# Optimization experiments

Hardware: AMD Instinct MI355X
Metric: run time of the kernel (lower is better)

## Reference

```python
import jax, jax.numpy as jnp
import numpy as np

KERNEL_SIZE = 3
STRIDE = 1

def setup_inputs() -> dict:
    key = jax.random.key(0)
    kx, kw, kb = jax.random.split(key, 3)
    B, C_in, L = 32, 64, 16384
    C_out = 64
    x = jax.random.normal(kx, (B, C_in, L), dtype=jnp.float32)
    # original uses torch.rand (uniform [0,1)) for params
    weight = jax.random.uniform(kw, (C_out, C_in, KERNEL_SIZE), dtype=jnp.float32)
    bias = jax.random.uniform(kb, (C_out,), dtype=jnp.float32)
    return {"x": x, "weight": weight, "bias": bias}

def reference(x, weight, bias):
    # x: (B, C_in, L), weight: (C_out, C_in, K) -> out: (B, C_out, L_out)
    out = jax.lax.conv_general_dilated(
        x, weight,
        window_strides=(STRIDE,),
        padding="VALID",
        dimension_numbers=("NCH", "OIH", "NCH"),
    )
    return out + bias[None, :, None]
```

## Files before the change

### kernel.cpp

```cpp
#include <hip/hip_runtime.h>


typedef __bf16 bf16x8 __attribute__((ext_vector_type(8)));
typedef unsigned short ushort8 __attribute__((ext_vector_type(8)));
typedef float f32x16 __attribute__((ext_vector_type(16)));

#define C_IN 64
#define C_OUT 64
#define L_IN 16384
#define L_OUT 16382
#define NT 256
#define PX 264
#define PW 200

__device__ __forceinline__ unsigned short f2bf(float f) {
  unsigned u = __builtin_bit_cast(unsigned, f);
  return (unsigned short)((u + 0x7FFFu + ((u >> 16) & 1u)) >> 16);
}

__global__ __launch_bounds__(256, 2) void conv1d_mfma(
    const float* __restrict__ x, const float* __restrict__ w,
    const float* __restrict__ bias, float* __restrict__ out) {
  __shared__ __align__(16) unsigned short xs[C_IN * PX];
  __shared__ __align__(16) unsigned short wl[C_OUT * PW];
  __shared__ float bias_s[C_OUT];

  const int t = threadIdx.x;
  const int bx = blockIdx.x;
  const int b = bx >> 6;
  const int tile = bx & 63;
  const int l0 = tile * NT;

  for (int i = t; i < C_OUT * 192; i += 256) {
    int co = i / 192;
    int r = i - co * 192;
    wl[co * PW + r] = f2bf(w[i]);
  }
  if (t < C_OUT) bias_s[t] = bias[t];

  {
    const int tj = t & 63;
    const int tc = t >> 6;
    const float* xb = x + (size_t)b * C_IN * L_IN + l0;
    for (int ci = tc; ci < C_IN; ci += 4) {
      const float* xr = xb + (size_t)ci * L_IN;
#pragma unroll
      for (int j0 = 0; j0 < 320; j0 += 64) {
        int j = j0 + tj;
        if (j < NT + 2) {
          float v = 0.0f;
          if (l0 + j < L_IN) v = xr[j];
          xs[ci * PX + j] = f2bf(v);
        }
      }
    }
  }
  __syncthreads();

  const int lane = t & 63;
  const int wv = t >> 6;
  const int half = lane >> 5;
  const int ln = lane & 31;
  const int n0 = wv * 64 + ln;
  const int kh = half * 8;

  f32x16 acc00 = {}, acc01 = {}, acc10 = {}, acc11 = {};

#pragma unroll
  for (int s = 0; s < 12; ++s) {
    bf16x8 a0 = *(const bf16x8*)&wl[ln * PW + s * 16 + kh];
    bf16x8 a1 = *(const bf16x8*)&wl[(32 + ln) * PW + s * 16 + kh];
    ushort8 b0u, b1u;
#pragma unroll
    for (int jj = 0; jj < 8; ++jj) {
      unsigned k = (unsigned)(s * 16 + kh + jj);
      unsigned ci = (k * 0xAAABu) >> 17;
      unsigned kk = k - ci * 3u;
      int base = (int)(ci * PX + kk) + n0;
      b0u[jj] = xs[base];
      b1u[jj] = xs[base + 32];
    }
    bf16x8 b0 = __builtin_bit_cast(bf16x8, b0u);
    bf16x8 b1 = __builtin_bit_cast(bf16x8, b1u);
    acc00 = __builtin_amdgcn_mfma_f32_32x32x16_bf16(a0, b0, acc00, 0, 0, 0);
    acc01 = __builtin_amdgcn_mfma_f32_32x32x16_bf16(a0, b1, acc01, 0, 0, 0);
    acc10 = __builtin_amdgcn_mfma_f32_32x32x16_bf16(a1, b0, acc10, 0, 0, 0);
    acc11 = __builtin_amdgcn_mfma_f32_32x32x16_bf16(a1, b1, acc11, 0, 0, 0);
  }

  const int l_base = l0 + wv * 64 + ln;
  const bool full = (l0 + NT <= L_OUT);
  if (full) {
#pragma unroll
    for (int mt = 0; mt < 2; ++mt) {
#pragma unroll
      for (int r = 0; r < 16; ++r) {
        int co = mt * 32 + 4 * half + (r & 3) + 8 * (r >> 2);
        float bv = bias_s[co];
        size_t row = ((size_t)b * C_OUT + co) * (size_t)L_OUT;
        float v0 = (mt == 0 ? acc00[r] : acc10[r]) + bv;
        float v1 = (mt == 0 ? acc01[r] : acc11[r]) + bv;
        out[row + l_base] = v0;
        out[row + l_base + 32] = v1;
      }
    }
  } else {
#pragma unroll
    for (int mt = 0; mt < 2; ++mt) {
#pragma unroll
      for (int r = 0; r < 16; ++r) {
        int co = mt * 32 + 4 * half + (r & 3) + 8 * (r >> 2);
        float bv = bias_s[co];
        size_t row = ((size_t)b * C_OUT + co) * (size_t)L_OUT;
        float v0 = (mt == 0 ? acc00[r] : acc10[r]) + bv;
        float v1 = (mt == 0 ? acc01[r] : acc11[r]) + bv;
        if (l_base < L_OUT) out[row + l_base] = v0;
        if (l_base + 32 < L_OUT) out[row + l_base + 32] = v1;
      }
    }
  }
}

extern "C" void kernel_launch(void* const* d_in, const int* in_sizes, int n_in,
                              void* d_out, int out_size, void* d_ws, size_t ws_size,
                              hipStream_t stream) {
  const float* x = (const float*)d_in[0];
  const float* w = (const float*)d_in[1];
  const float* bias = (const float*)d_in[2];
  float* out = (float*)d_out;
  conv1d_mfma<<<dim3(32 * 64), dim3(256), 0, stream>>>(x, w, bias, out);
}
```

Measured before the change: 304.9 us.

## Load conv input directly from global memory, dropping the shared-memory x tile

Removes the LDS staging of the input tile and instead has each lane read fp32 x values straight from global memory, converting them to bf16 in registers for the MFMA B operand. The weight layout in LDS is reordered to (kk, ci) so each k-slice maps to a fixed tap offset and 8 consecutive channels. The LDS footprint shrinks, so launch bounds are raised to 4 blocks per CU. The cost is 16 scattered scalar global loads per MFMA step, and the roughly 3x reuse of each input element across taps now has to come from L1/L2 instead of LDS.

```diff
diff --git a/kernel.cpp b/kernel.cpp
--- a/kernel.cpp
+++ b/kernel.cpp
@@ -10,7 +10,6 @@
 #define L_IN 16384
 #define L_OUT 16382
 #define NT 256
-#define PX 264
 #define PW 200
 
 __device__ __forceinline__ unsigned short f2bf(float f) {
@@ -18,10 +17,9 @@
   return (unsigned short)((u + 0x7FFFu + ((u >> 16) & 1u)) >> 16);
 }
 
-__global__ __launch_bounds__(256, 2) void conv1d_mfma(
+__global__ __launch_bounds__(256, 4) void conv1d_mfma(
     const float* __restrict__ x, const float* __restrict__ w,
     const float* __restrict__ bias, float* __restrict__ out) {
-  __shared__ __align__(16) unsigned short xs[C_IN * PX];
   __shared__ __align__(16) unsigned short wl[C_OUT * PW];
   __shared__ float bias_s[C_OUT];
 
@@ -34,35 +32,22 @@
   for (int i = t; i < C_OUT * 192; i += 256) {
     int co = i / 192;
     int r = i - co * 192;
-    wl[co * PW + r] = f2bf(w[i]);
+    int ci = r / 3;
+    int kk = r - ci * 3;
+    wl[co * PW + kk * 64 + ci] = f2bf(w[i]);
   }
   if (t < C_OUT) bias_s[t] = bias[t];
-
-  {
-    const int tj = t & 63;
-    const int tc = t >> 6;
-    const float* xb = x + (size_t)b * C_IN * L_IN + l0;
-    for (int ci = tc; ci < C_IN; ci += 4) {
-      const float* xr = xb + (size_t)ci * L_IN;
-#pragma unroll
-      for (int j0 = 0; j0 < 320; j0 += 64) {
-        int j = j0 + tj;
-        if (j < NT + 2) {
-          float v = 0.0f;
-          if (l0 + j < L_IN) v = xr[j];
-          xs[ci * PX + j] = f2bf(v);
-        }
-      }
-    }
-  }
   __syncthreads();
 
   const int lane = t & 63;
   const int wv = t >> 6;
   const int half = lane >> 5;
   const int ln = lane & 31;
+  const int kh = half * 8;
   const int n0 = wv * 64 + ln;
-  const int kh = half * 8;
+  const int l_a = l0 + n0;
+
+  const float* xb = x + (size_t)b * (C_IN * L_IN);
 
   f32x16 acc00 = {}, acc01 = {}, acc10 = {}, acc11 = {};
 
@@ -70,15 +55,18 @@
   for (int s = 0; s < 12; ++s) {
     bf16x8 a0 = *(const bf16x8*)&wl[ln * PW + s * 16 + kh];
     bf16x8 a1 = *(const bf16x8*)&wl[(32 + ln) * PW + s * 16 + kh];
+
+    int tt = s * 16 + kh;
+    int kk = tt >> 6;
+    int ci0 = tt & 63;
+    int p0 = min(l_a + kk, L_IN - 1);
+    int p1 = min(l_a + 32 + kk, L_IN - 1);
+    int base = ci0 * L_IN;
     ushort8 b0u, b1u;
 #pragma unroll
     for (int jj = 0; jj < 8; ++jj) {
-      unsigned k = (unsigned)(s * 16 + kh + jj);
-      unsigned ci = (k * 0xAAABu) >> 17;
-      unsigned kk = k - ci * 3u;
-      int base = (int)(ci * PX + kk) + n0;
-      b0u[jj] = xs[base];
-      b1u[jj] = xs[base + 32];
+      b0u[jj] = f2bf(xb[base + jj * L_IN + p0]);
+      b1u[jj] = f2bf(xb[base + jj * L_IN + p1]);
     }
     bf16x8 b0 = __builtin_bit_cast(bf16x8, b0u);
     bf16x8 b1 = __builtin_bit_cast(bf16x8, b1u);
```

Result: faster. 283.9 us (-6.9%).
